# Kernel optimization log

Measured on AMD Instinct MI355X. Metric: run time of the kernel, lower is better.

## Reference

```python
import jax, jax.numpy as jnp
import numpy as np

B, N, K = 8, 512, 16            # batches, proposals per batch, knn neighbors
C_POOL = 256                    # pooled feature dim (hardcoded 256 in source)
G_MLP = [128, 128]              # GLOBAL_INFORMATION.MLP_LAYERS
IN_DIM = C_POOL + G_MLP[-1]     # gnn_input_dim = 384
LAYERS = [512, 512, 512]


def _xavier(key, shape):
    fan_out, fan_in = shape
    lim = np.sqrt(6.0 / (fan_in + fan_out))
    return jax.random.uniform(key, shape, jnp.float32, -lim, lim)


def setup_inputs() -> dict:
    key = jax.random.key(0)
    ks = jax.random.split(key, 12)
    rois = jax.random.normal(ks[0], (B, N, 7), jnp.float32)
    rois = rois.at[:, :, :3].multiply(20.0)  # spread box centers spatially
    pooled_features = jax.random.normal(ks[1], (B, N, C_POOL), jnp.float32)

    # knn_graph per batch (loop=False): edges (neighbor j -> center i)
    coords = rois[:, :, :3]
    d2 = jnp.sum((coords[:, :, None, :] - coords[:, None, :, :]) ** 2, -1)  # [B,N,N]
    d2 = d2 + jnp.eye(N, dtype=jnp.float32) * 1e9                           # no self loops
    _, nbr = jax.lax.top_k(-d2, K)                                          # [B,N,K]
    offs = (jnp.arange(B) * N)[:, None, None]
    src = (nbr + offs).reshape(-1)
    dst = (jnp.broadcast_to(jnp.arange(N)[None, :, None], (B, N, K)) + offs).reshape(-1)
    edge_index = jnp.stack([src, dst]).astype(jnp.int32)                    # [2, B*N*K]

    # global-information MLP params: Linear(7,128), Linear(128,128)
    gW1 = _xavier(ks[2], (G_MLP[0], 7)); gb1 = jnp.zeros((G_MLP[0],), jnp.float32)
    gW2 = _xavier(ks[3], (G_MLP[1], G_MLP[0])); gb2 = jnp.zeros((G_MLP[1],), jnp.float32)

    # EdgeConv fc params: in = 2*in_dim of layer
    fcW1 = _xavier(ks[4], (LAYERS[0], 2 * IN_DIM)); fcb1 = jnp.zeros((LAYERS[0],), jnp.float32)
    fcW2 = _xavier(ks[5], (LAYERS[1], 2 * LAYERS[0])); fcb2 = jnp.zeros((LAYERS[1],), jnp.float32)
    fcW3 = _xavier(ks[6], (LAYERS[2], 2 * LAYERS[1])); fcb3 = jnp.zeros((LAYERS[2],), jnp.float32)

    return dict(rois=rois, pooled_features=pooled_features, edge_index=edge_index,
                gW1=gW1, gb1=gb1, gW2=gW2, gb2=gb2,
                fcW1=fcW1, fcb1=fcb1, fcW2=fcW2, fcb2=fcb2, fcW3=fcW3, fcb3=fcb3)


def reference(rois, pooled_features, edge_index,
              gW1, gb1, gW2, gb2,
              fcW1, fcb1, fcW2, fcb2, fcW3, fcb3):
    # global information MLP on proposal boxes
    g = jax.nn.relu(rois @ gW1.T + gb1)
    g = jax.nn.relu(g @ gW2.T + gb2)                      # [B,N,128]
    x = jnp.concatenate([pooled_features, g], -1).reshape(-1, IN_DIM)  # [B*N, 384]

    src, dst = edge_index[0], edge_index[1]
    n_nodes = B * N
    feats = [x]
    for W, b in ((fcW1, fcb1), (fcW2, fcb2), (fcW3, fcb3)):
        x_i = x[dst]                                      # target features [E,d]
        x_j = x[src]                                      # source features [E,d]
        msg = jax.nn.relu(jnp.concatenate([x_j - x_i, x_i], -1) @ W.T + b)  # [E,out]
        x = jax.ops.segment_max(msg, dst, num_segments=n_nodes)  # scatter-max aggr
        feats.append(x)
    return jnp.concatenate(feats, -1)                     # [B*N, 384+512*3]
```

## Files before the change

kernel.cpp:

```cpp
#include <hip/hip_runtime.h>
#include <hip/hip_bf16.h>

#define BN_NODES 4096
#define KNN 16
#define C_POOL 256
#define G_DIM 128
#define IN_DIM 384
#define L_DIM 512
#define OUT_STRIDE 1920

#define X0_OFF 0
#define X1_OFF 384
#define X2_OFF 896
#define X3_OFF 1408

typedef __attribute__((ext_vector_type(8))) __bf16 bf16x8;
typedef __attribute__((ext_vector_type(4))) float floatx4;

static __device__ __forceinline__ ushort f2bf(float v) {
  return __builtin_bit_cast(ushort, __float2bfloat16(v));
}
static __device__ __forceinline__ float bf2f(ushort u) {
  return __builtin_bit_cast(float, ((unsigned)u) << 16);
}

__global__ __launch_bounds__(128) void node_feat_kernel(
    const float* __restrict__ rois, const float* __restrict__ pooled,
    const float* __restrict__ gW1, const float* __restrict__ gb1,
    const float* __restrict__ gW2, const float* __restrict__ gb2,
    float* __restrict__ out, ushort* __restrict__ Xb) {
  int n = blockIdx.x;
  int t = threadIdx.x;
  __shared__ float r[7];
  __shared__ __align__(16) float h1[G_DIM];
  if (t < 7) r[t] = rois[(size_t)n * 7 + t];
  __syncthreads();
  float acc = gb1[t];
#pragma unroll
  for (int i = 0; i < 7; i++) acc += r[i] * gW1[t * 7 + i];
  h1[t] = fmaxf(acc, 0.f);
  __syncthreads();
  float acc2 = gb2[t];
  const float4* w4 = (const float4*)(gW2 + (size_t)t * G_DIM);
  const float4* h4 = (const float4*)h1;
#pragma unroll 8
  for (int i = 0; i < G_DIM / 4; i++) {
    float4 wv = w4[i];
    float4 hv = h4[i];
    acc2 += wv.x * hv.x + wv.y * hv.y + wv.z * hv.z + wv.w * hv.w;
  }
  float g = fmaxf(acc2, 0.f);
  float* orow = out + (size_t)n * OUT_STRIDE;
  const float* prow = pooled + (size_t)n * C_POOL;
  float p0 = prow[t], p1 = prow[G_DIM + t];
  orow[t] = p0;
  orow[G_DIM + t] = p1;
  orow[C_POOL + t] = g;
  ushort* xrow = Xb + (size_t)n * IN_DIM;
  xrow[t] = f2bf(p0);
  xrow[G_DIM + t] = f2bf(p1);
  xrow[C_POOL + t] = f2bf(g);
}

__global__ __launch_bounds__(128) void wconv_all_kernel(
    const float* __restrict__ W0, const float* __restrict__ W1,
    const float* __restrict__ W2, ushort* __restrict__ Wb0,
    ushort* __restrict__ Wb1, ushort* __restrict__ Wb2) {
  int l = blockIdx.z;
  int j = blockIdx.y;
  int k = blockIdx.x * 128 + threadIdx.x;
  int K = (l == 0) ? IN_DIM : L_DIM;
  if (k >= K) return;
  const float* W = (l == 0) ? W0 : (l == 1) ? W1 : W2;
  ushort* Wb = (l == 0) ? Wb0 : (l == 1) ? Wb1 : Wb2;
  float v = (j < 512) ? W[(size_t)j * (2 * K) + k]
                      : W[(size_t)(j - 512) * (2 * K) + K + k];
  Wb[(size_t)j * K + k] = f2bf(v);
}

__global__ __launch_bounds__(256) void mfma_gemm_kernel(
    const ushort* __restrict__ Xb, const ushort* __restrict__ Wb, int K,
    ushort* __restrict__ PQb) {
  __shared__ ushort sA[128 * 32];
  __shared__ ushort sB[64 * 32];
  const int tid = threadIdx.x;
  const int lane = tid & 63;
  const int w = tid >> 6;
  const int wm = w >> 1;
  const int wn = w & 1;
  const int fr = lane & 15;
  const int quad = lane >> 4;
  const int srow = lane >> 2;
  const int scol = (lane & 3) * 8;

  floatx4 acc[4][2];
#pragma unroll
  for (int i = 0; i < 4; i++)
#pragma unroll
    for (int j = 0; j < 2; j++) acc[i][j] = (floatx4){0.f, 0.f, 0.f, 0.f};

  const size_t aBase = (size_t)blockIdx.x * 128 + w * 32;
  const size_t bBase = (size_t)blockIdx.y * 64 + w * 16;

  for (int k0 = 0; k0 < K; k0 += 32) {
#pragma unroll
    for (int p = 0; p < 2; p++) {
      const ushort* ga = Xb + (aBase + p * 16 + srow) * K + (k0 + scol);
      __builtin_amdgcn_global_load_lds(
          (const __attribute__((address_space(1))) void*)ga,
          (__attribute__((address_space(3))) void*)&sA[(w * 32 + p * 16) * 32],
          16, 0, 0);
    }
    {
      const ushort* gb = Wb + (bBase + srow) * K + (k0 + scol);
      __builtin_amdgcn_global_load_lds(
          (const __attribute__((address_space(1))) void*)gb,
          (__attribute__((address_space(3))) void*)&sB[(w * 16) * 32],
          16, 0, 0);
    }
    __syncthreads();
    bf16x8 af[4], bfr[2];
#pragma unroll
    for (int i = 0; i < 4; i++)
      af[i] = *(const bf16x8*)&sA[(wm * 64 + i * 16 + fr) * 32 + quad * 8];
#pragma unroll
    for (int j = 0; j < 2; j++)
      bfr[j] = *(const bf16x8*)&sB[(wn * 32 + j * 16 + fr) * 32 + quad * 8];
#pragma unroll
    for (int i = 0; i < 4; i++)
#pragma unroll
      for (int j = 0; j < 2; j++)
        acc[i][j] = __builtin_amdgcn_mfma_f32_16x16x32_bf16(af[i], bfr[j],
                                                            acc[i][j], 0, 0, 0);
    __syncthreads();
  }

  const int rowB = blockIdx.x * 128 + wm * 64 + quad * 4;
  const int colB = blockIdx.y * 64 + wn * 32 + fr;
#pragma unroll
  for (int i = 0; i < 4; i++)
#pragma unroll
    for (int j = 0; j < 2; j++)
#pragma unroll
      for (int r = 0; r < 4; r++)
        PQb[(size_t)(rowB + i * 16 + r) * 1024 + colB + j * 16] =
            f2bf(acc[i][j][r]);
}

__global__ __launch_bounds__(128) void edge_kernel(
    const ushort* __restrict__ PQb, const int* __restrict__ src,
    const float* __restrict__ bias, float* __restrict__ out, int out_off,
    ushort* __restrict__ Xb) {
  int n = blockIdx.x;
  int t = threadIdx.x;
  __shared__ int s[KNN];
  if (t < KNN) s[t] = src[n * KNN + t];
  __syncthreads();
  const ushort* row = PQb + (size_t)n * 1024;
  ushort4 pu = *(const ushort4*)(row + t * 4);
  ushort4 qu = *(const ushort4*)(row + 512 + t * 4);
  float4 bb = ((const float4*)bias)[t];
  float bx = bf2f(qu.x) - bf2f(pu.x) + bb.x;
  float by = bf2f(qu.y) - bf2f(pu.y) + bb.y;
  float bz = bf2f(qu.z) - bf2f(pu.z) + bb.z;
  float bw = bf2f(qu.w) - bf2f(pu.w) + bb.w;
  float mx = -1e30f, my = -1e30f, mz = -1e30f, mw = -1e30f;
#pragma unroll
  for (int k = 0; k < KNN; k++) {
    ushort4 u = *(const ushort4*)(PQb + (size_t)s[k] * 1024 + t * 4);
    mx = fmaxf(mx, bf2f(u.x));
    my = fmaxf(my, bf2f(u.y));
    mz = fmaxf(mz, bf2f(u.z));
    mw = fmaxf(mw, bf2f(u.w));
  }
  float4 res;
  res.x = fmaxf(mx + bx, 0.f);
  res.y = fmaxf(my + by, 0.f);
  res.z = fmaxf(mz + bz, 0.f);
  res.w = fmaxf(mw + bw, 0.f);
  float* orow = out + (size_t)n * OUT_STRIDE + out_off;
  ((float4*)orow)[t] = res;
  ushort4 pk;
  pk.x = f2bf(res.x);
  pk.y = f2bf(res.y);
  pk.z = f2bf(res.z);
  pk.w = f2bf(res.w);
  ((ushort4*)(Xb + (size_t)n * L_DIM))[t] = pk;
}

extern "C" void kernel_launch(void* const* d_in, const int* in_sizes, int n_in,
                              void* d_out, int out_size, void* d_ws,
                              size_t ws_size, hipStream_t stream) {
  const float* rois = (const float*)d_in[0];
  const float* pooled = (const float*)d_in[1];
  const int* edge_index = (const int*)d_in[2];
  const float* gW1 = (const float*)d_in[3];
  const float* gb1 = (const float*)d_in[4];
  const float* gW2 = (const float*)d_in[5];
  const float* gb2 = (const float*)d_in[6];
  const float* fcW[3] = {(const float*)d_in[7], (const float*)d_in[9],
                         (const float*)d_in[11]};
  const float* fcb[3] = {(const float*)d_in[8], (const float*)d_in[10],
                         (const float*)d_in[12]};
  float* out = (float*)d_out;
  const int* src = edge_index;

  char* ws = (char*)d_ws;
  ushort* PQb = (ushort*)ws;
  ushort* Xb = (ushort*)(ws + (size_t)8 * 1024 * 1024);
  ushort* Wb[3] = {(ushort*)(ws + (size_t)12 * 1024 * 1024),
                   (ushort*)(ws + (size_t)13 * 1024 * 1024),
                   (ushort*)(ws + (size_t)14 * 1024 * 1024)};

  wconv_all_kernel<<<dim3(4, 1024, 3), 128, 0, stream>>>(
      fcW[0], fcW[1], fcW[2], Wb[0], Wb[1], Wb[2]);
  node_feat_kernel<<<BN_NODES, 128, 0, stream>>>(rois, pooled, gW1, gb1, gW2,
                                                 gb2, out, Xb);

  const int out_off[3] = {X1_OFF, X2_OFF, X3_OFF};
  const int Kdim[3] = {IN_DIM, L_DIM, L_DIM};

  for (int l = 0; l < 3; l++) {
    mfma_gemm_kernel<<<dim3(32, 16), 256, 0, stream>>>(Xb, Wb[l], Kdim[l],
                                                       PQb);
    edge_kernel<<<BN_NODES, 128, 0, stream>>>(PQb, src, fcb[l], out,
                                              out_off[l], Xb);
  }
}
```

Baseline: 190.6 us.

## Batch node MLP over 8 nodes per block and deepen GEMM K-tile to 64

After: 177.6 us. 6.8% less time.

```diff
diff --git a/kernel.cpp b/kernel.cpp
--- a/kernel.cpp
+++ b/kernel.cpp
@@ -24,42 +24,64 @@
   return __builtin_bit_cast(float, ((unsigned)u) << 16);
 }
 
-__global__ __launch_bounds__(128) void node_feat_kernel(
+__global__ __launch_bounds__(256) void node_feat_kernel(
     const float* __restrict__ rois, const float* __restrict__ pooled,
     const float* __restrict__ gW1, const float* __restrict__ gb1,
     const float* __restrict__ gW2, const float* __restrict__ gb2,
     float* __restrict__ out, ushort* __restrict__ Xb) {
-  int n = blockIdx.x;
-  int t = threadIdx.x;
-  __shared__ float r[7];
-  __shared__ __align__(16) float h1[G_DIM];
-  if (t < 7) r[t] = rois[(size_t)n * 7 + t];
+  const int nb = blockIdx.x * 8;
+  const int t = threadIdx.x;
+  const int c = t & 127;
+  const int nh = t >> 7;
+  __shared__ float rs[8 * 7];
+  __shared__ __align__(16) float h1[8][G_DIM];
+  if (t < 56) rs[t] = rois[(size_t)nb * 7 + t];
   __syncthreads();
-  float acc = gb1[t];
-#pragma unroll
-  for (int i = 0; i < 7; i++) acc += r[i] * gW1[t * 7 + i];
-  h1[t] = fmaxf(acc, 0.f);
+  {
+    float w1[7];
+#pragma unroll
+    for (int i = 0; i < 7; i++) w1[i] = gW1[c * 7 + i];
+    float b1 = gb1[c];
+#pragma unroll
+    for (int n = nh * 4; n < nh * 4 + 4; n++) {
+      float a = b1;
+#pragma unroll
+      for (int i = 0; i < 7; i++) a += rs[n * 7 + i] * w1[i];
+      h1[n][c] = fmaxf(a, 0.f);
+    }
+  }
   __syncthreads();
-  float acc2 = gb2[t];
-  const float4* w4 = (const float4*)(gW2 + (size_t)t * G_DIM);
-  const float4* h4 = (const float4*)h1;
-#pragma unroll 8
-  for (int i = 0; i < G_DIM / 4; i++) {
-    float4 wv = w4[i];
-    float4 hv = h4[i];
-    acc2 += wv.x * hv.x + wv.y * hv.y + wv.z * hv.z + wv.w * hv.w;
-  }
-  float g = fmaxf(acc2, 0.f);
-  float* orow = out + (size_t)n * OUT_STRIDE;
-  const float* prow = pooled + (size_t)n * C_POOL;
-  float p0 = prow[t], p1 = prow[G_DIM + t];
-  orow[t] = p0;
-  orow[G_DIM + t] = p1;
-  orow[C_POOL + t] = g;
-  ushort* xrow = Xb + (size_t)n * IN_DIM;
-  xrow[t] = f2bf(p0);
-  xrow[G_DIM + t] = f2bf(p1);
-  xrow[C_POOL + t] = f2bf(g);
+  float acc[4];
+  {
+    float b2 = gb2[c];
+#pragma unroll
+    for (int n = 0; n < 4; n++) acc[n] = b2;
+    const float4* w4 = (const float4*)(gW2 + (size_t)c * G_DIM);
+#pragma unroll 4
+    for (int kc = 0; kc < G_DIM / 4; kc++) {
+      float4 wv = w4[kc];
+#pragma unroll
+      for (int n = 0; n < 4; n++) {
+        float4 hv = ((const float4*)h1[nh * 4 + n])[kc];
+        acc[n] += wv.x * hv.x + wv.y * hv.y + wv.z * hv.z + wv.w * hv.w;
+      }
+    }
+  }
+#pragma unroll
+  for (int n = 0; n < 4; n++) {
+    int node = nb + nh * 4 + n;
+    float g = fmaxf(acc[n], 0.f);
+    const float* prow = pooled + (size_t)node * C_POOL;
+    float p0 = prow[c], p1 = prow[G_DIM + c];
+    float* orow = out + (size_t)node * OUT_STRIDE;
+    orow[c] = p0;
+    orow[G_DIM + c] = p1;
+    orow[C_POOL + c] = g;
+    ushort* xrow = Xb + (size_t)node * IN_DIM;
+    xrow[c] = f2bf(p0);
+    xrow[G_DIM + c] = f2bf(p1);
+    xrow[C_POOL + c] = f2bf(g);
+  }
 }
 
 __global__ __launch_bounds__(128) void wconv_all_kernel(
@@ -81,17 +103,15 @@
 __global__ __launch_bounds__(256) void mfma_gemm_kernel(
     const ushort* __restrict__ Xb, const ushort* __restrict__ Wb, int K,
     ushort* __restrict__ PQb) {
-  __shared__ ushort sA[128 * 32];
-  __shared__ ushort sB[64 * 32];
+  __shared__ ushort sA[128 * 64];
+  __shared__ ushort sB[64 * 64];
   const int tid = threadIdx.x;
   const int lane = tid & 63;
   const int w = tid >> 6;
-  const int wm = w >> 1;
-  const int wn = w & 1;
+  const int wm = w >> 1, wn = w & 1;
   const int fr = lane & 15;
-  const int quad = lane >> 4;
-  const int srow = lane >> 2;
-  const int scol = (lane & 3) * 8;
+  const int kc = lane >> 4;
+  const int bm = blockIdx.x, bn = blockIdx.y;
 
   floatx4 acc[4][2];
 #pragma unroll
@@ -99,44 +119,52 @@
 #pragma unroll
     for (int j = 0; j < 2; j++) acc[i][j] = (floatx4){0.f, 0.f, 0.f, 0.f};
 
-  const size_t aBase = (size_t)blockIdx.x * 128 + w * 32;
-  const size_t bBase = (size_t)blockIdx.y * 64 + w * 16;
-
-  for (int k0 = 0; k0 < K; k0 += 32) {
-#pragma unroll
-    for (int p = 0; p < 2; p++) {
-      const ushort* ga = Xb + (aBase + p * 16 + srow) * K + (k0 + scol);
+  for (int k0 = 0; k0 < K; k0 += 64) {
+#pragma unroll
+    for (int r = 0; r < 4; r++) {
+      int t = w + r * 4;
+      int rt = t & 7, ks = t >> 3;
+      const ushort* ga =
+          Xb + (size_t)(bm * 128 + rt * 16 + fr) * K + k0 + ks * 32 + kc * 8;
       __builtin_amdgcn_global_load_lds(
           (const __attribute__((address_space(1))) void*)ga,
-          (__attribute__((address_space(3))) void*)&sA[(w * 32 + p * 16) * 32],
-          16, 0, 0);
-    }
-    {
-      const ushort* gb = Wb + (bBase + srow) * K + (k0 + scol);
+          (__attribute__((address_space(3))) void*)&sA[t * 512 + lane * 8], 16,
+          0, 0);
+    }
+#pragma unroll
+    for (int r = 0; r < 2; r++) {
+      int t = w + r * 4;
+      int ct = t & 3, ks = t >> 2;
+      const ushort* gb =
+          Wb + (size_t)(bn * 64 + ct * 16 + fr) * K + k0 + ks * 32 + kc * 8;
       __builtin_amdgcn_global_load_lds(
           (const __attribute__((address_space(1))) void*)gb,
-          (__attribute__((address_space(3))) void*)&sB[(w * 16) * 32],
-          16, 0, 0);
+          (__attribute__((address_space(3))) void*)&sB[t * 512 + lane * 8], 16,
+          0, 0);
     }
     __syncthreads();
-    bf16x8 af[4], bfr[2];
-#pragma unroll
-    for (int i = 0; i < 4; i++)
-      af[i] = *(const bf16x8*)&sA[(wm * 64 + i * 16 + fr) * 32 + quad * 8];
-#pragma unroll
-    for (int j = 0; j < 2; j++)
-      bfr[j] = *(const bf16x8*)&sB[(wn * 32 + j * 16 + fr) * 32 + quad * 8];
-#pragma unroll
-    for (int i = 0; i < 4; i++)
+#pragma unroll
+    for (int ks = 0; ks < 2; ks++) {
+      bf16x8 af[4], bf[2];
+#pragma unroll
+      for (int i = 0; i < 4; i++)
+        af[i] = *(const bf16x8*)&sA[(ks * 8 + wm * 4 + i) * 512 + lane * 8];
 #pragma unroll
       for (int j = 0; j < 2; j++)
-        acc[i][j] = __builtin_amdgcn_mfma_f32_16x16x32_bf16(af[i], bfr[j],
-                                                            acc[i][j], 0, 0, 0);
+        bf[j] = *(const bf16x8*)&sB[(ks * 4 + wn * 2 + j) * 512 + lane * 8];
+#pragma unroll
+      for (int i = 0; i < 4; i++)
+#pragma unroll
+        for (int j = 0; j < 2; j++)
+          acc[i][j] = __builtin_amdgcn_mfma_f32_16x16x32_bf16(af[i], bf[j],
+                                                              acc[i][j], 0, 0,
+                                                              0);
+    }
     __syncthreads();
   }
 
-  const int rowB = blockIdx.x * 128 + wm * 64 + quad * 4;
-  const int colB = blockIdx.y * 64 + wn * 32 + fr;
+  const int rowB = bm * 128 + wm * 64 + kc * 4;
+  const int colB = bn * 64 + wn * 32 + fr;
 #pragma unroll
   for (int i = 0; i < 4; i++)
 #pragma unroll
@@ -214,8 +242,8 @@
 
   wconv_all_kernel<<<dim3(4, 1024, 3), 128, 0, stream>>>(
       fcW[0], fcW[1], fcW[2], Wb[0], Wb[1], Wb[2]);
-  node_feat_kernel<<<BN_NODES, 128, 0, stream>>>(rois, pooled, gW1, gb1, gW2,
-                                                 gb2, out, Xb);
+  node_feat_kernel<<<BN_NODES / 8, 256, 0, stream>>>(rois, pooled, gW1, gb1,
+                                                     gW2, gb2, out, Xb);
 
   const int out_off[3] = {X1_OFF, X2_OFF, X3_OFF};
   const int Kdim[3] = {IN_DIM, L_DIM, L_DIM};
```
